# Kernel optimization log

Measured on AMD Instinct MI355X. Metric: run time of the kernel, lower is better.

## Reference

```python
import jax, jax.numpy as jnp
import numpy as np

K = 1024
D = 64
BETA = 0.25


def setup_inputs() -> dict:
    key = jax.random.key(0)
    k1, k2 = jax.random.split(key)
    latents = jax.random.normal(k1, (32, 64, 64, 64), dtype=jnp.float32)  # [B, C=D, H, W]
    # embedding init: uniform(-1/K, 1/K)
    embedding = jax.random.uniform(k2, (K, D), dtype=jnp.float32, minval=-1.0 / K, maxval=1.0 / K)
    return {"latents": latents, "embedding": embedding}


def reference(latents, embedding):
    # [B, D, H, W] -> [B, H, W, D]
    x = jnp.transpose(latents, (0, 2, 3, 1))
    shp = x.shape
    flat = x.reshape(-1, D)  # [N, D]

    dist = (jnp.sum(flat ** 2, axis=1, keepdims=True)
            + jnp.sum(embedding ** 2, axis=1)
            - 2.0 * flat @ embedding.T)  # [N, K]
    inds = jnp.argmin(dist, axis=1)  # [N]

    quantized = embedding[inds].reshape(shp)  # gather == one-hot @ embedding

    commitment_loss = jnp.mean((jax.lax.stop_gradient(quantized) - x) ** 2)
    embedding_loss = jnp.mean((quantized - jax.lax.stop_gradient(x)) ** 2)
    vq_loss = commitment_loss * BETA + embedding_loss

    # straight-through estimator
    quantized = x + jax.lax.stop_gradient(quantized - x)
    out = jnp.transpose(quantized, (0, 3, 1, 2))  # back to [B, D, H, W]
    return out, vq_loss
```

## Files before the change

### kernel.cpp

```cpp
#include <hip/hip_runtime.h>
#include <hip/hip_bf16.h>


#define HW 4096
#define OUTELEMS 8388608

typedef __attribute__((ext_vector_type(8))) short bf16x8;
typedef __attribute__((ext_vector_type(4))) float f32x4;
typedef __attribute__((ext_vector_type(4))) int i32x4;

static __device__ __forceinline__ short f2bf(float f) {
    union { __hip_bfloat16 h; short s; } u;
    u.h = __float2bfloat16(f);
    return u.s;
}
static __device__ __forceinline__ unsigned umin2(unsigned a, unsigned b) {
    return a < b ? a : b;
}


__global__ __launch_bounds__(256) void prep_kernel(const float* __restrict__ emb,
                                                   short* __restrict__ Ebf,
                                                   float* __restrict__ en1,
                                                   float* __restrict__ loss) {
    int code = blockIdx.x * 4 + (threadIdx.x >> 6);
    int d = threadIdx.x & 63;
    float v = emb[code * 64 + d];
    int g = d >> 3, j = d & 7;
    Ebf[code * 64 + ((g + code) & 7) * 8 + j] = f2bf(-2.0f * v);
    float s = v * v;
#pragma unroll
    for (int off = 32; off > 0; off >>= 1) s += __shfl_xor(s, off, 64);
    if (d == 0) en1[code] = 1.0f + s;
    if (blockIdx.x == 0 && threadIdx.x == 0) *loss = 0.0f;
}

__global__ __launch_bounds__(1024, 4) void vq_kernel(
        const float* __restrict__ lat, const short* __restrict__ Ebf,
        const float* __restrict__ en1, float* __restrict__ out,
        float* __restrict__ loss) {
    extern __shared__ __align__(16) char sbuf[];
    const int tid  = threadIdx.x;
    const int wave = tid >> 6;
    const int lane = tid & 63;
    const int n    = lane & 15;
    const int quad = lane >> 4;

    const int g0 = blockIdx.x * 512;
    const int b  = g0 >> 12;
    const int mb = g0 & 4095;
    const float* latb = lat + (size_t)b * 262144;

    {
        const f32x4* src = (const f32x4*)Ebf;
        f32x4* dst = (f32x4*)sbuf;
#pragma unroll
        for (int r = 0; r < 8; ++r)
            dst[r * 1024 + tid] = src[r * 1024 + tid];
        if (tid < 256)
            ((f32x4*)(sbuf + 131072))[tid] = ((const f32x4*)en1)[tid];
    }

    bf16x8 bfr[2][2];
    float xnorm[2];
#pragma unroll
    for (int s = 0; s < 2; ++s) {
        const float* xp = latb + (mb + wave * 32 + s * 16 + n);
        float xs = 0.0f; bf16x8 f0, f1;
#pragma unroll
        for (int j = 0; j < 8; ++j) {
            float x0 = xp[(quad * 8 + j) * HW];
            float x1 = xp[(32 + quad * 8 + j) * HW];
            xs += x0 * x0 + x1 * x1;
            f0[j] = f2bf(x0); f1[j] = f2bf(x1);
        }
        bfr[s][0] = f0; bfr[s][1] = f1; xnorm[s] = xs;
    }
    __syncthreads();

    const int slot0 = ((quad + n) & 7) * 16;
    const int slot1 = ((quad + 4 + n) & 7) * 16;
    const char* arowBase = sbuf + n * 128;
    const f32x4* enl = (const f32x4*)(sbuf + 131072);
    unsigned emin[2] = {0xFFFFFFFFu, 0xFFFFFFFFu};

#pragma unroll 2
    for (int ct = 0; ct < 64; ++ct) {
        const char* rb = arowBase + ct * 2048;
        bf16x8 a0 = *(const bf16x8*)(rb + slot0);
        bf16x8 a1 = *(const bf16x8*)(rb + slot1);
        f32x4 en4 = enl[ct * 4 + quad];
        const unsigned cb = ct * 16 + quad * 4;
#pragma unroll
        for (int s = 0; s < 2; ++s) {
            f32x4 acc = __builtin_amdgcn_mfma_f32_16x16x32_bf16(a0, bfr[s][0], en4, 0, 0, 0);
            acc = __builtin_amdgcn_mfma_f32_16x16x32_bf16(a1, bfr[s][1], acc, 0, 0, 0);
            unsigned e0 = (__float_as_uint(acc[0]) & 0xFFFFFC00u) | (cb + 0);
            unsigned e1 = (__float_as_uint(acc[1]) & 0xFFFFFC00u) | (cb + 1);
            unsigned e2 = (__float_as_uint(acc[2]) & 0xFFFFFC00u) | (cb + 2);
            unsigned e3 = (__float_as_uint(acc[3]) & 0xFFFFFC00u) | (cb + 3);
            emin[s] = umin2(umin2(umin2(umin2(e0, e1), e2), e3), emin[s]);
        }
    }

#pragma unroll
    for (int off = 16; off <= 32; off <<= 1) {
#pragma unroll
        for (int s = 0; s < 2; ++s) {
            unsigned eo = (unsigned)__shfl_xor((int)emin[s], off, 64);
            float xo = __shfl_xor(xnorm[s], off, 64);
            emin[s] = eo < emin[s] ? eo : emin[s];
            xnorm[s] += xo;
        }
    }

    int* codes = (int*)(sbuf + 135168);
    if (quad == 0) {
        codes[wave * 32 + n]      = (int)(emin[0] & 1023u);
        codes[wave * 32 + 16 + n] = (int)(emin[1] & 1023u);
    }

    float contrib = 0.0f;
#pragma unroll
    for (int s = 0; s < 2; ++s)
        contrib += __uint_as_float(emin[s] & 0xFFFFFC00u) - 1.0f + xnorm[s];
#pragma unroll
    for (int off = 32; off > 0; off >>= 1) contrib += __shfl_xor(contrib, off, 64);
    float* wsum = (float*)(sbuf + 137216);
    if (lane == 0) wsum[wave] = contrib;
    __syncthreads();

    float* outb = out + (size_t)b * 262144 + mb;
#pragma unroll 2
    for (int i = 0; i < 4; ++i) {
        int id = i * 1024 + tid;
        int dp = id >> 7;
        int d  = dp * 2;
        int mq = (id & 127) * 4;
        i32x4 c4 = *(const i32x4*)(codes + mq);
        int g = d >> 3, j2 = (d & 7) * 2;
        unsigned u0 = *(const unsigned*)(sbuf + c4.x * 128 + ((g + c4.x) & 7) * 16 + j2);
        unsigned u1 = *(const unsigned*)(sbuf + c4.y * 128 + ((g + c4.y) & 7) * 16 + j2);
        unsigned u2 = *(const unsigned*)(sbuf + c4.z * 128 + ((g + c4.z) & 7) * 16 + j2);
        unsigned u3 = *(const unsigned*)(sbuf + c4.w * 128 + ((g + c4.w) & 7) * 16 + j2);
        f32x4 vlo, vhi;
        vlo[0] = __uint_as_float(u0 << 16) * -0.5f;
        vlo[1] = __uint_as_float(u1 << 16) * -0.5f;
        vlo[2] = __uint_as_float(u2 << 16) * -0.5f;
        vlo[3] = __uint_as_float(u3 << 16) * -0.5f;
        vhi[0] = __uint_as_float(u0 & 0xFFFF0000u) * -0.5f;
        vhi[1] = __uint_as_float(u1 & 0xFFFF0000u) * -0.5f;
        vhi[2] = __uint_as_float(u2 & 0xFFFF0000u) * -0.5f;
        vhi[3] = __uint_as_float(u3 & 0xFFFF0000u) * -0.5f;
        *(f32x4*)(outb + d * HW + mq)       = vlo;
        *(f32x4*)(outb + (d + 1) * HW + mq) = vhi;
    }

    if (tid == 0) {
        float t = 0.0f;
#pragma unroll
        for (int w = 0; w < 16; ++w) t += wsum[w];
        atomicAdd(loss, t * (1.25f / (8388608.0f * 4.0f)));
    }
}

extern "C" void kernel_launch(void* const* d_in, const int* in_sizes, int n_in,
                              void* d_out, int out_size, void* d_ws, size_t ws_size,
                              hipStream_t stream) {
    const float* latents   = (const float*)d_in[0];
    const float* embedding = (const float*)d_in[1];
    float* out  = (float*)d_out;
    float* loss = out + OUTELEMS;

    char* ws = (char*)d_ws;
    short* Ebf = (short*)ws;
    float* en1 = (float*)(ws + 131072);

    hipFuncSetAttribute((const void*)vq_kernel,
                        hipFuncAttributeMaxDynamicSharedMemorySize, 137280);

    prep_kernel<<<256, 256, 0, stream>>>(embedding, Ebf, en1, loss);
    vq_kernel<<<256, 1024, 137280, stream>>>(latents, Ebf, en1, out, loss);
}
```

Before: 104.4 us.

## Split codebook across wave pairs to reuse LDS code fragments over more positions

Each pair of waves now shares 64 positions, with each wave scanning half of the codebook and holding four position tiles in registers instead of two. This doubles how many MFMAs each LDS-loaded code fragment feeds and halves the loop trip count per wave. Partial argmins are merged through shared-memory atomicMin on packed distance|index keys, and the loss is summed per position. This adds an extra barrier and shared atomics, and raises register pressure from the larger fragment arrays.

```diff
diff --git a/kernel.cpp b/kernel.cpp
--- a/kernel.cpp
+++ b/kernel.cpp
@@ -45,11 +45,17 @@
     const int lane = tid & 63;
     const int n    = lane & 15;
     const int quad = lane >> 4;
+    const int pr   = wave >> 1;
+    const int half = wave & 1;
 
     const int g0 = blockIdx.x * 512;
     const int b  = g0 >> 12;
     const int mb = g0 & 4095;
     const float* latb = lat + (size_t)b * 262144;
+
+    unsigned* enc = (unsigned*)(sbuf + 135168);
+    float* xn     = (float*)(sbuf + 137216);
+    float* wsum   = (float*)(sbuf + 139264);
 
     {
         const f32x4* src = (const f32x4*)Ebf;
@@ -59,13 +65,14 @@
             dst[r * 1024 + tid] = src[r * 1024 + tid];
         if (tid < 256)
             ((f32x4*)(sbuf + 131072))[tid] = ((const f32x4*)en1)[tid];
+        if (tid < 512) enc[tid] = 0xFFFFFFFFu;
     }
 
-    bf16x8 bfr[2][2];
-    float xnorm[2];
+    bf16x8 bfr[4][2];
+    float xnorm[4];
 #pragma unroll
-    for (int s = 0; s < 2; ++s) {
-        const float* xp = latb + (mb + wave * 32 + s * 16 + n);
+    for (int s = 0; s < 4; ++s) {
+        const float* xp = latb + (mb + pr * 64 + s * 16 + n);
         float xs = 0.0f; bf16x8 f0, f1;
 #pragma unroll
         for (int j = 0; j < 8; ++j) {
@@ -80,19 +87,20 @@
 
     const int slot0 = ((quad + n) & 7) * 16;
     const int slot1 = ((quad + 4 + n) & 7) * 16;
-    const char* arowBase = sbuf + n * 128;
-    const f32x4* enl = (const f32x4*)(sbuf + 131072);
-    unsigned emin[2] = {0xFFFFFFFFu, 0xFFFFFFFFu};
+    const char* arowBase = sbuf + n * 128 + half * 65536;
+    const f32x4* enl = (const f32x4*)(sbuf + 131072) + half * 128;
+    const unsigned cbb = half * 512;
+    unsigned emin[4] = {0xFFFFFFFFu, 0xFFFFFFFFu, 0xFFFFFFFFu, 0xFFFFFFFFu};
 
 #pragma unroll 2
-    for (int ct = 0; ct < 64; ++ct) {
+    for (int ct = 0; ct < 32; ++ct) {
         const char* rb = arowBase + ct * 2048;
         bf16x8 a0 = *(const bf16x8*)(rb + slot0);
         bf16x8 a1 = *(const bf16x8*)(rb + slot1);
         f32x4 en4 = enl[ct * 4 + quad];
-        const unsigned cb = ct * 16 + quad * 4;
+        const unsigned cb = cbb + ct * 16 + quad * 4;
 #pragma unroll
-        for (int s = 0; s < 2; ++s) {
+        for (int s = 0; s < 4; ++s) {
             f32x4 acc = __builtin_amdgcn_mfma_f32_16x16x32_bf16(a0, bfr[s][0], en4, 0, 0, 0);
             acc = __builtin_amdgcn_mfma_f32_16x16x32_bf16(a1, bfr[s][1], acc, 0, 0, 0);
             unsigned e0 = (__float_as_uint(acc[0]) & 0xFFFFFC00u) | (cb + 0);
@@ -106,7 +114,7 @@
 #pragma unroll
     for (int off = 16; off <= 32; off <<= 1) {
 #pragma unroll
-        for (int s = 0; s < 2; ++s) {
+        for (int s = 0; s < 4; ++s) {
             unsigned eo = (unsigned)__shfl_xor((int)emin[s], off, 64);
             float xo = __shfl_xor(xnorm[s], off, 64);
             emin[s] = eo < emin[s] ? eo : emin[s];
@@ -114,21 +122,25 @@
         }
     }
 
-    int* codes = (int*)(sbuf + 135168);
     if (quad == 0) {
-        codes[wave * 32 + n]      = (int)(emin[0] & 1023u);
-        codes[wave * 32 + 16 + n] = (int)(emin[1] & 1023u);
+#pragma unroll
+        for (int s = 0; s < 4; ++s)
+            atomicMin(&enc[pr * 64 + s * 16 + n], emin[s]);
+        if (half == 0) {
+#pragma unroll
+            for (int s = 0; s < 4; ++s)
+                xn[pr * 64 + s * 16 + n] = xnorm[s];
+        }
     }
+    __syncthreads();
 
-    float contrib = 0.0f;
+    if (tid < 512) {
+        unsigned e = enc[tid];
+        float c = __uint_as_float(e & 0xFFFFFC00u) - 1.0f + xn[tid];
 #pragma unroll
-    for (int s = 0; s < 2; ++s)
-        contrib += __uint_as_float(emin[s] & 0xFFFFFC00u) - 1.0f + xnorm[s];
-#pragma unroll
-    for (int off = 32; off > 0; off >>= 1) contrib += __shfl_xor(contrib, off, 64);
-    float* wsum = (float*)(sbuf + 137216);
-    if (lane == 0) wsum[wave] = contrib;
-    __syncthreads();
+        for (int off = 32; off > 0; off >>= 1) c += __shfl_xor(c, off, 64);
+        if (lane == 0) wsum[wave] = c;
+    }
 
     float* outb = out + (size_t)b * 262144 + mb;
 #pragma unroll 2
@@ -137,12 +149,13 @@
         int dp = id >> 7;
         int d  = dp * 2;
         int mq = (id & 127) * 4;
-        i32x4 c4 = *(const i32x4*)(codes + mq);
+        i32x4 c4 = *(const i32x4*)(enc + mq);
+        int cx = c4.x & 1023, cy = c4.y & 1023, cz = c4.z & 1023, cw = c4.w & 1023;
         int g = d >> 3, j2 = (d & 7) * 2;
-        unsigned u0 = *(const unsigned*)(sbuf + c4.x * 128 + ((g + c4.x) & 7) * 16 + j2);
-        unsigned u1 = *(const unsigned*)(sbuf + c4.y * 128 + ((g + c4.y) & 7) * 16 + j2);
-        unsigned u2 = *(const unsigned*)(sbuf + c4.z * 128 + ((g + c4.z) & 7) * 16 + j2);
-        unsigned u3 = *(const unsigned*)(sbuf + c4.w * 128 + ((g + c4.w) & 7) * 16 + j2);
+        unsigned u0 = *(const unsigned*)(sbuf + cx * 128 + ((g + cx) & 7) * 16 + j2);
+        unsigned u1 = *(const unsigned*)(sbuf + cy * 128 + ((g + cy) & 7) * 16 + j2);
+        unsigned u2 = *(const unsigned*)(sbuf + cz * 128 + ((g + cz) & 7) * 16 + j2);
+        unsigned u3 = *(const unsigned*)(sbuf + cw * 128 + ((g + cw) & 7) * 16 + j2);
         f32x4 vlo, vhi;
         vlo[0] = __uint_as_float(u0 << 16) * -0.5f;
         vlo[1] = __uint_as_float(u1 << 16) * -0.5f;
@@ -156,11 +169,12 @@
         *(f32x4*)(outb + (d + 1) * HW + mq) = vhi;
     }
 
+    __syncthreads();
     if (tid == 0) {
         float t = 0.0f;
 #pragma unroll
-        for (int w = 0; w < 16; ++w) t += wsum[w];
-        atomicAdd(loss, t * (1.25f / (8388608.0f * 4.0f)));
+        for (int w = 0; w < 8; ++w) t += wsum[w];
+        atomicAdd(loss, t * (1.25f / 8388608.0f));
     }
 }
 
@@ -177,8 +191,8 @@
     float* en1 = (float*)(ws + 131072);
 
     hipFuncSetAttribute((const void*)vq_kernel,
-                        hipFuncAttributeMaxDynamicSharedMemorySize, 137280);
+                        hipFuncAttributeMaxDynamicSharedMemorySize, 139328);
 
     prep_kernel<<<256, 256, 0, stream>>>(embedding, Ebf, en1, loss);
-    vq_kernel<<<256, 1024, 137280, stream>>>(latents, Ebf, en1, out, loss);
+    vq_kernel<<<256, 1024, 139328, stream>>>(latents, Ebf, en1, out, loss);
 }
```

After: 105.8 us. Within noise of the previous version (+1.3%).
